# Performance work log

Hardware: AMD Instinct MI355X
Metric: run time of the kernel (lower is better)

The kernel has to match this reference:

```python
import jax, jax.numpy as jnp
import numpy as np

N = 100000
E = 1200000


def _gcn_norm(edge_index, num_nodes):
    # Add self-loops and compute symmetric normalization (PyG GCNConv default).
    row = jnp.concatenate([edge_index[0], jnp.arange(num_nodes, dtype=edge_index.dtype)])
    col = jnp.concatenate([edge_index[1], jnp.arange(num_nodes, dtype=edge_index.dtype)])
    deg = jax.ops.segment_sum(jnp.ones_like(col, dtype=jnp.float32), col, num_segments=num_nodes)
    dinv = jnp.where(deg > 0, jax.lax.rsqrt(jnp.maximum(deg, 1.0)), 0.0)
    norm = dinv[row] * dinv[col]  # [E+N]
    return row, col, norm


def _gcn_conv(x, W, b, row, col, norm, num_nodes):
    h = x @ W                      # [N, out] dense transform first (fewer bytes to gather)
    msg = h[row] * norm[:, None]   # gather + edge-wise scale
    out = jax.ops.segment_sum(msg, col, num_segments=num_nodes)  # scatter-add to targets
    return out + b


def setup_inputs() -> dict:
    key = jax.random.key(0)
    k1, k2, k3, k4 = jax.random.split(key, 4)
    x = jax.random.normal(k1, (N, 128), dtype=jnp.float32)
    edge_index = jax.random.randint(k2, (2, E), 0, N, dtype=jnp.int64)
    W1 = jax.random.normal(k3, (128, 256), dtype=jnp.float32) * (1.0 / np.sqrt(128))
    b1 = jnp.zeros((256,), dtype=jnp.float32)
    W2 = jax.random.normal(k4, (256, 40), dtype=jnp.float32) * (1.0 / np.sqrt(256))
    b2 = jnp.zeros((40,), dtype=jnp.float32)
    return {"x": x, "edge_index": edge_index, "W1": W1, "b1": b1, "W2": W2, "b2": b2}


def reference(x, edge_index, W1, b1, W2, b2):
    row, col, norm = _gcn_norm(edge_index, N)
    h = _gcn_conv(x, W1, b1, row, col, norm, N)
    h = jax.nn.relu(h)
    # dropout omitted: eval mode (training=False) is identity
    return _gcn_conv(h, W2, b2, row, col, norm, N)
```

## Files before the change

### kernel.cpp

```cpp
#include <hip/hip_runtime.h>
#include <hip/hip_bf16.h>

#define NN 100000
#define EE 1200000
#define F1 128
#define F2 256
#define F3 40
#define MROWS 64
#define NBUK ((NN + 255) / 256)
#define NBLK 256
#define CHUNK ((EE + NBLK - 1) / NBLK)
#define DCAP 4096
#define WB ((F1 * F2 + F2 * 48 + 255) / 256)

typedef __bf16 bf16x8 __attribute__((ext_vector_type(8)));
typedef float  f32x4  __attribute__((ext_vector_type(4)));

__device__ __forceinline__ unsigned short f2bf(float f) {
    unsigned u = __float_as_uint(f);
    return (unsigned short)((u + 0x7fffu + ((u >> 16) & 1u)) >> 16);
}
__device__ __forceinline__ float bflo(unsigned v) { return __uint_as_float(v << 16); }
__device__ __forceinline__ float bfhi(unsigned v) { return __uint_as_float(v & 0xffff0000u); }

__global__ __launch_bounds__(256) void k_hist(const int* __restrict__ col,
                                              int* __restrict__ hist) {
    __shared__ int lh[NBUK];
    for (int i = threadIdx.x; i < NBUK; i += 256) lh[i] = 0;
    __syncthreads();
    int e0 = blockIdx.x * CHUNK;
    int e1 = min(e0 + CHUNK, EE);
    for (int e = e0 + threadIdx.x * 4; e + 3 < e1; e += 1024) {
        int4 c = *(const int4*)(col + e);
        if ((unsigned)c.x < (unsigned)NN) atomicAdd(&lh[c.x >> 8], 1);
        if ((unsigned)c.y < (unsigned)NN) atomicAdd(&lh[c.y >> 8], 1);
        if ((unsigned)c.z < (unsigned)NN) atomicAdd(&lh[c.z >> 8], 1);
        if ((unsigned)c.w < (unsigned)NN) atomicAdd(&lh[c.w >> 8], 1);
    }
    __syncthreads();
    for (int i = threadIdx.x; i < NBUK; i += 256) hist[blockIdx.x * NBUK + i] = lh[i];
}

__global__ __launch_bounds__(256) void k_scanbin(int* __restrict__ hist,
                                                 int* __restrict__ bintot) {
    __shared__ int s[NBLK];
    int b = blockIdx.x;
    int v = hist[threadIdx.x * NBUK + b];
    s[threadIdx.x] = v;
    __syncthreads();
    int acc = v;
    for (int d = 1; d < NBLK; d <<= 1) {
        int add = (threadIdx.x >= d) ? s[threadIdx.x - d] : 0;
        __syncthreads();
        acc += add;
        s[threadIdx.x] = acc;
        __syncthreads();
    }
    hist[threadIdx.x * NBUK + b] = acc - v;
    if (threadIdx.x == NBLK - 1) bintot[b] = acc;
}

__global__ __launch_bounds__(512) void k_scanbase(const int* __restrict__ bintot,
                                                  int* __restrict__ binbase) {
    __shared__ int s[512];
    int v = (threadIdx.x < NBUK) ? bintot[threadIdx.x] : 0;
    s[threadIdx.x] = v;
    __syncthreads();
    int acc = v;
    for (int d = 1; d < 512; d <<= 1) {
        int add = (threadIdx.x >= d) ? s[threadIdx.x - d] : 0;
        __syncthreads();
        acc += add;
        s[threadIdx.x] = acc;
        __syncthreads();
    }
    if (threadIdx.x < NBUK) binbase[threadIdx.x] = acc - v;
    if (threadIdx.x == NBUK - 1) binbase[NBUK] = acc;
}

__global__ __launch_bounds__(256) void k_scat(const int* __restrict__ row,
                                              const int* __restrict__ col,
                                              const int* __restrict__ hist,
                                              const int* __restrict__ binbase,
                                              unsigned* __restrict__ rec) {
    __shared__ int lcur[NBUK];
    for (int i = threadIdx.x; i < NBUK; i += 256)
        lcur[i] = binbase[i] + hist[blockIdx.x * NBUK + i];
    __syncthreads();
    int e0 = blockIdx.x * CHUNK;
    int e1 = min(e0 + CHUNK, EE);
    for (int e = e0 + threadIdx.x * 4; e + 3 < e1; e += 1024) {
        int4 r = *(const int4*)(row + e);
        int4 c = *(const int4*)(col + e);
        if ((unsigned)c.x < (unsigned)NN) {
            int p = atomicAdd(&lcur[c.x >> 8], 1);
            rec[p] = ((unsigned)r.x & 0xFFFFFFu) | ((unsigned)(c.x & 255) << 24);
        }
        if ((unsigned)c.y < (unsigned)NN) {
            int p = atomicAdd(&lcur[c.y >> 8], 1);
            rec[p] = ((unsigned)r.y & 0xFFFFFFu) | ((unsigned)(c.y & 255) << 24);
        }
        if ((unsigned)c.z < (unsigned)NN) {
            int p = atomicAdd(&lcur[c.z >> 8], 1);
            rec[p] = ((unsigned)r.z & 0xFFFFFFu) | ((unsigned)(c.z & 255) << 24);
        }
        if ((unsigned)c.w < (unsigned)NN) {
            int p = atomicAdd(&lcur[c.w >> 8], 1);
            rec[p] = ((unsigned)r.w & 0xFFFFFFu) | ((unsigned)(c.w & 255) << 24);
        }
    }
}

__global__ __launch_bounds__(256) void k_csr(const int* __restrict__ binbase,
                                             const unsigned* __restrict__ rec,
                                             int* __restrict__ eidx,
                                             int* __restrict__ cnt,
                                             int* __restrict__ cursor,
                                             float* __restrict__ dinv,
                                             const float4* __restrict__ x4,
                                             unsigned* __restrict__ xh,
                                             const float* __restrict__ W1,
                                             const float* __restrict__ W2,
                                             __hip_bfloat16* __restrict__ W1p,
                                             __hip_bfloat16* __restrict__ W2p) {
    if (blockIdx.x >= NBUK) {
        int idx = (blockIdx.x - NBUK) * 256 + threadIdx.x;
        if (idx < F1 * F2) {
            int k = idx / F2, colw = idx - (idx / F2) * F2;
            int k8 = k >> 3, j = k & 7;
            W1p[((size_t)(k8 * F2 + colw) << 3) + j] = __float2bfloat16(W1[(size_t)k * F2 + colw]);
        } else if (idx < F1 * F2 + F2 * 48) {
            int i2 = idx - F1 * F2;
            int k = i2 / 48, colw = i2 - (i2 / 48) * 48;
            int k8 = k >> 3, j = k & 7;
            float v = (colw < F3) ? W2[(size_t)k * F3 + colw] : 0.0f;
            W2p[((size_t)(k8 * 48 + colw) << 3) + j] = __float2bfloat16(v);
        }
        return;
    }
    __shared__ int lcnt[256];
    __shared__ int s[256];
    __shared__ int lcur[256];
    __shared__ float sdinv[256];
    __shared__ int lde[DCAP];
    const int b = blockIdx.x;
    const int tid = threadIdx.x;
    lcnt[tid] = 0;
    __syncthreads();
    const int base = binbase[b];
    const int nb = min(binbase[b + 1] - base, DCAP);
    for (int j = tid; j < nb; j += 256) atomicAdd(&lcnt[rec[base + j] >> 24], 1);
    __syncthreads();
    int cv = lcnt[tid];
    s[tid] = cv;
    __syncthreads();
    int acc = cv;
    for (int d = 1; d < 256; d <<= 1) {
        int add = (tid >= d) ? s[tid - d] : 0;
        __syncthreads();
        acc += add;
        s[tid] = acc;
        __syncthreads();
    }
    int excl = acc - cv;
    lcur[tid] = excl;
    const int node = (b << 8) + tid;
    float dv = rsqrtf((float)(cv + 1));
    sdinv[tid] = dv;
    if (node < NN) {
        cnt[node] = cv;
        cursor[node] = base + excl + cv;
        dinv[node] = dv;
    }
    __syncthreads();
    for (int j = tid; j < nb; j += 256) {
        unsigned v = rec[base + j];
        int pos = atomicAdd(&lcur[v >> 24], 1);
        lde[pos] = (int)(v & 0xFFFFFFu);
    }
    __syncthreads();
    for (int j = tid; j < nb; j += 256) eidx[base + j] = lde[j];
    for (int j = tid; j < 256 * 32; j += 256) {
        int nl = j >> 5;
        int gn = (b << 8) + nl;
        if (gn < NN) {
            float d = sdinv[nl];
            float4 v = x4[(size_t)gn * 32 + (j & 31)];
            uint2 o;
            o.x = (unsigned)f2bf(v.x * d) | ((unsigned)f2bf(v.y * d) << 16);
            o.y = (unsigned)f2bf(v.z * d) | ((unsigned)f2bf(v.w * d) << 16);
            *(uint2*)(xh + ((size_t)gn << 6) + ((j & 31) << 1)) = o;
        }
    }
}

__global__ __launch_bounds__(256) void k_agg1(const int* __restrict__ cursor,
                                              const int* __restrict__ cnt,
                                              const int* __restrict__ eidx,
                                              const float* __restrict__ dinv,
                                              const unsigned* __restrict__ xh,
                                              unsigned* __restrict__ agg) {
    int node = blockIdx.x * 4 + (threadIdx.x >> 6);
    int lane = threadIdx.x & 63;
    if (node >= NN) return;
    const int g = lane >> 4;
    const int l = lane & 15;
    float a0, a1, a2, a3, a4, a5, a6, a7;
    {
        uint4 v = {0u, 0u, 0u, 0u};
        if (g == 0) v = *(const uint4*)(xh + ((size_t)node << 6) + (l << 2));
        a0 = bflo(v.x); a1 = bfhi(v.x); a2 = bflo(v.y); a3 = bfhi(v.y);
        a4 = bflo(v.z); a5 = bfhi(v.z); a6 = bflo(v.w); a7 = bfhi(v.w);
    }
    int n = cnt[node];
    int s = cursor[node] - n;
    int k = 0;
    for (; k + 7 < n; k += 8) {
        int r0 = eidx[s + k + g];
        int r1 = eidx[s + k + 4 + g];
        uint4 v0 = *(const uint4*)(xh + ((size_t)r0 << 6) + (l << 2));
        uint4 v1 = *(const uint4*)(xh + ((size_t)r1 << 6) + (l << 2));
        a0 += bflo(v0.x); a1 += bfhi(v0.x); a2 += bflo(v0.y); a3 += bfhi(v0.y);
        a4 += bflo(v0.z); a5 += bfhi(v0.z); a6 += bflo(v0.w); a7 += bfhi(v0.w);
        a0 += bflo(v1.x); a1 += bfhi(v1.x); a2 += bflo(v1.y); a3 += bfhi(v1.y);
        a4 += bflo(v1.z); a5 += bfhi(v1.z); a6 += bflo(v1.w); a7 += bfhi(v1.w);
    }
    for (; k < n; k += 4) {
        if (k + g < n) {
            int r0 = eidx[s + k + g];
            uint4 v0 = *(const uint4*)(xh + ((size_t)r0 << 6) + (l << 2));
            a0 += bflo(v0.x); a1 += bfhi(v0.x); a2 += bflo(v0.y); a3 += bfhi(v0.y);
            a4 += bflo(v0.z); a5 += bfhi(v0.z); a6 += bflo(v0.w); a7 += bfhi(v0.w);
        }
    }
    a0 += __shfl_down(a0, 32, 64); a1 += __shfl_down(a1, 32, 64);
    a2 += __shfl_down(a2, 32, 64); a3 += __shfl_down(a3, 32, 64);
    a4 += __shfl_down(a4, 32, 64); a5 += __shfl_down(a5, 32, 64);
    a6 += __shfl_down(a6, 32, 64); a7 += __shfl_down(a7, 32, 64);
    a0 += __shfl_down(a0, 16, 64); a1 += __shfl_down(a1, 16, 64);
    a2 += __shfl_down(a2, 16, 64); a3 += __shfl_down(a3, 16, 64);
    a4 += __shfl_down(a4, 16, 64); a5 += __shfl_down(a5, 16, 64);
    a6 += __shfl_down(a6, 16, 64); a7 += __shfl_down(a7, 16, 64);
    if (g == 0) {
        float d = dinv[node];
        uint4 o;
        o.x = (unsigned)f2bf(a0 * d) | ((unsigned)f2bf(a1 * d) << 16);
        o.y = (unsigned)f2bf(a2 * d) | ((unsigned)f2bf(a3 * d) << 16);
        o.z = (unsigned)f2bf(a4 * d) | ((unsigned)f2bf(a5 * d) << 16);
        o.w = (unsigned)f2bf(a6 * d) | ((unsigned)f2bf(a7 * d) << 16);
        *(uint4*)(agg + ((size_t)node << 6) + (l << 2)) = o;
    }
}

__global__ __launch_bounds__(256) void k_gemm_mfma(
    const __hip_bfloat16* __restrict__ agg, const __hip_bfloat16* __restrict__ W1p,
    const float* __restrict__ b1, const __hip_bfloat16* __restrict__ W2p,
    const float* __restrict__ dinv, unsigned short* __restrict__ tg) {
    __shared__ __hip_bfloat16 h_s[MROWS][F2 + 8];
    const int i0   = blockIdx.x * MROWS;
    const int wave = threadIdx.x >> 6;
    const int lane = threadIdx.x & 63;
    const int m = lane & 15, q = lane >> 4;
    const int rowA = i0 + wave * 16 + m;

    f32x4 acc[16];
#pragma unroll
    for (int c = 0; c < 16; ++c) acc[c] = (f32x4){0.f, 0.f, 0.f, 0.f};

#pragma unroll
    for (int s = 0; s < 4; ++s) {
        bf16x8 a;
#pragma unroll
        for (int j = 0; j < 8; ++j) a[j] = (__bf16)0.0f;
        if (rowA < NN) a = *(const bf16x8*)(agg + (size_t)rowA * F1 + s * 32 + q * 8);
        const __hip_bfloat16* bp = W1p + ((size_t)(4 * s + q) * F2) * 8;
#pragma unroll
        for (int c = 0; c < 16; ++c) {
            bf16x8 b = *(const bf16x8*)(bp + ((size_t)(c * 16 + m) << 3));
            acc[c] = __builtin_amdgcn_mfma_f32_16x16x32_bf16(a, b, acc[c], 0, 0, 0);
        }
    }

#pragma unroll
    for (int c = 0; c < 16; ++c) {
        int col = c * 16 + m;
        float bj = b1[col];
#pragma unroll
        for (int r = 0; r < 4; ++r) {
            int lr = wave * 16 + q * 4 + r;
            h_s[lr][col] = __float2bfloat16(fmaxf(acc[c][r] + bj, 0.0f));
        }
    }
    __syncthreads();

    f32x4 acc2[3];
#pragma unroll
    for (int c = 0; c < 3; ++c) acc2[c] = (f32x4){0.f, 0.f, 0.f, 0.f};

#pragma unroll
    for (int s = 0; s < 8; ++s) {
        bf16x8 a = *(const bf16x8*)(&h_s[wave * 16 + m][s * 32 + q * 8]);
        const __hip_bfloat16* bp = W2p + ((size_t)(4 * s + q) * 48) * 8;
#pragma unroll
        for (int c = 0; c < 3; ++c) {
            bf16x8 b = *(const bf16x8*)(bp + ((size_t)(c * 16 + m) << 3));
            acc2[c] = __builtin_amdgcn_mfma_f32_16x16x32_bf16(a, b, acc2[c], 0, 0, 0);
        }
    }

#pragma unroll
    for (int c = 0; c < 3; ++c) {
        int col = c * 16 + m;
        if (col < F3) {
#pragma unroll
            for (int r = 0; r < 4; ++r) {
                int grow = i0 + wave * 16 + q * 4 + r;
                if (grow < NN)
                    tg[((size_t)grow << 6) + col] = f2bf(acc2[c][r] * dinv[grow]);
            }
        }
    }
}

__global__ __launch_bounds__(256) void k_agg2(const int* __restrict__ cursor,
                                              const int* __restrict__ cnt,
                                              const int* __restrict__ eidx,
                                              const float* __restrict__ dinv,
                                              const unsigned* __restrict__ tg32,
                                              const float* __restrict__ b2,
                                              float* __restrict__ out) {
    int node = blockIdx.x * 4 + (threadIdx.x >> 6);
    int lane = threadIdx.x & 63;
    if (node >= NN) return;
    const int g = lane / 20;
    const int l = lane - g * 20;
    const bool act = g < 3;
    float a0 = 0.f, a1 = 0.f;
    if (g == 0) {
        unsigned v = tg32[((size_t)node << 5) + l];
        a0 = bflo(v); a1 = bfhi(v);
    }
    int n = cnt[node];
    int s = cursor[node] - n;
    int k = 0;
    for (; k + 5 < n; k += 6) {
        unsigned v0 = 0u, v1 = 0u;
        if (act) {
            int r0 = eidx[s + k + g];
            int r1 = eidx[s + k + 3 + g];
            v0 = tg32[((size_t)r0 << 5) + l];
            v1 = tg32[((size_t)r1 << 5) + l];
        }
        a0 += bflo(v0); a1 += bfhi(v0);
        a0 += bflo(v1); a1 += bfhi(v1);
    }
    for (; k < n; k += 3) {
        if (act && (k + g) < n) {
            int r0 = eidx[s + k + g];
            unsigned v0 = tg32[((size_t)r0 << 5) + l];
            a0 += bflo(v0); a1 += bfhi(v0);
        }
    }
    float t0a = __shfl_down(a0, 20, 64), t0b = __shfl_down(a0, 40, 64);
    float t1a = __shfl_down(a1, 20, 64), t1b = __shfl_down(a1, 40, 64);
    if (lane < 20) {
        float d = dinv[node];
        float o0 = d * (a0 + t0a + t0b) + b2[2 * lane];
        float o1 = d * (a1 + t1a + t1b) + b2[2 * lane + 1];
        float2 o = {o0, o1};
        *(float2*)(out + (size_t)node * F3 + (lane << 1)) = o;
    }
}

extern "C" void kernel_launch(void* const* d_in, const int* in_sizes, int n_in,
                              void* d_out, int out_size, void* d_ws, size_t ws_size,
                              hipStream_t stream) {
    const float* x  = (const float*)d_in[0];
    const int*   ei = (const int*)d_in[1];
    const float* W1 = (const float*)d_in[2];
    const float* b1 = (const float*)d_in[3];
    const float* W2 = (const float*)d_in[4];
    const float* b2 = (const float*)d_in[5];
    float* out = (float*)d_out;

    const int* row = ei;
    const int* col = ei + EE;

    int* cnt     = (int*)d_ws;
    int* cursor  = cnt + NN;
    float* dinv  = (float*)(cursor + NN);
    int* hist    = (int*)(dinv + NN);
    int* bintot  = hist + NBLK * NBUK;
    int* binbase = bintot + NBUK;
    int* eidx    = binbase + (NBUK + 1) + 7;
    unsigned* xh  = (unsigned*)(eidx + EE);
    unsigned* agg = xh + (size_t)NN * 64;
    unsigned* rec = agg;
    unsigned short* tg = (unsigned short*)xh;
    __hip_bfloat16* W1p = (__hip_bfloat16*)(agg + (size_t)NN * 64);
    __hip_bfloat16* W2p = W1p + (size_t)F1 * F2;

    k_hist    <<<NBLK, 256, 0, stream>>>(col, hist);
    k_scanbin <<<NBUK, NBLK, 0, stream>>>(hist, bintot);
    k_scanbase<<<1, 512, 0, stream>>>(bintot, binbase);
    k_scat    <<<NBLK, 256, 0, stream>>>(row, col, hist, binbase, rec);
    k_csr     <<<NBUK + WB, 256, 0, stream>>>(binbase, rec, eidx, cnt, cursor, dinv,
                                              (const float4*)x, xh, W1, W2, W1p, W2p);

    k_agg1<<<(NN + 3) / 4, 256, 0, stream>>>(cursor, cnt, eidx, dinv, xh, agg);
    k_gemm_mfma<<<(NN + MROWS - 1) / MROWS, 256, 0, stream>>>(
        (const __hip_bfloat16*)agg, W1p, b1, W2p, dinv, tg);
    k_agg2<<<(NN + 3) / 4, 256, 0, stream>>>(cursor, cnt, eidx, dinv,
                                             (const unsigned*)tg, b2, out);
}
```

Measured before the change: 306.1 us.

## Fuse first-layer aggregation into the MFMA GEMM kernel via shared memory

Merges the layer-1 neighbor aggregation kernel with the two-GEMM MFMA kernel. Each wave now aggregates its 16 rows sequentially into a shared-memory tile, and the GEMMs read that tile instead of a global agg buffer. This removes one launch and a full write and read of the aggregated feature matrix. In exchange, the gather phase runs in far fewer blocks and each wave walks 16 nodes serially, which may reduce memory-level parallelism and occupancy for the latency-bound gather. LDS use per block also goes up.

```diff
diff --git a/kernel.cpp b/kernel.cpp
--- a/kernel.cpp
+++ b/kernel.cpp
@@ -194,85 +194,84 @@
     }
 }
 
-__global__ __launch_bounds__(256) void k_agg1(const int* __restrict__ cursor,
-                                              const int* __restrict__ cnt,
-                                              const int* __restrict__ eidx,
-                                              const float* __restrict__ dinv,
-                                              const unsigned* __restrict__ xh,
-                                              unsigned* __restrict__ agg) {
-    int node = blockIdx.x * 4 + (threadIdx.x >> 6);
-    int lane = threadIdx.x & 63;
-    if (node >= NN) return;
-    const int g = lane >> 4;
-    const int l = lane & 15;
-    float a0, a1, a2, a3, a4, a5, a6, a7;
-    {
-        uint4 v = {0u, 0u, 0u, 0u};
-        if (g == 0) v = *(const uint4*)(xh + ((size_t)node << 6) + (l << 2));
-        a0 = bflo(v.x); a1 = bfhi(v.x); a2 = bflo(v.y); a3 = bfhi(v.y);
-        a4 = bflo(v.z); a5 = bfhi(v.z); a6 = bflo(v.w); a7 = bfhi(v.w);
-    }
-    int n = cnt[node];
-    int s = cursor[node] - n;
-    int k = 0;
-    for (; k + 7 < n; k += 8) {
-        int r0 = eidx[s + k + g];
-        int r1 = eidx[s + k + 4 + g];
-        uint4 v0 = *(const uint4*)(xh + ((size_t)r0 << 6) + (l << 2));
-        uint4 v1 = *(const uint4*)(xh + ((size_t)r1 << 6) + (l << 2));
-        a0 += bflo(v0.x); a1 += bfhi(v0.x); a2 += bflo(v0.y); a3 += bfhi(v0.y);
-        a4 += bflo(v0.z); a5 += bfhi(v0.z); a6 += bflo(v0.w); a7 += bfhi(v0.w);
-        a0 += bflo(v1.x); a1 += bfhi(v1.x); a2 += bflo(v1.y); a3 += bfhi(v1.y);
-        a4 += bflo(v1.z); a5 += bfhi(v1.z); a6 += bflo(v1.w); a7 += bfhi(v1.w);
-    }
-    for (; k < n; k += 4) {
-        if (k + g < n) {
-            int r0 = eidx[s + k + g];
-            uint4 v0 = *(const uint4*)(xh + ((size_t)r0 << 6) + (l << 2));
-            a0 += bflo(v0.x); a1 += bfhi(v0.x); a2 += bflo(v0.y); a3 += bfhi(v0.y);
-            a4 += bflo(v0.z); a5 += bfhi(v0.z); a6 += bflo(v0.w); a7 += bfhi(v0.w);
-        }
-    }
-    a0 += __shfl_down(a0, 32, 64); a1 += __shfl_down(a1, 32, 64);
-    a2 += __shfl_down(a2, 32, 64); a3 += __shfl_down(a3, 32, 64);
-    a4 += __shfl_down(a4, 32, 64); a5 += __shfl_down(a5, 32, 64);
-    a6 += __shfl_down(a6, 32, 64); a7 += __shfl_down(a7, 32, 64);
-    a0 += __shfl_down(a0, 16, 64); a1 += __shfl_down(a1, 16, 64);
-    a2 += __shfl_down(a2, 16, 64); a3 += __shfl_down(a3, 16, 64);
-    a4 += __shfl_down(a4, 16, 64); a5 += __shfl_down(a5, 16, 64);
-    a6 += __shfl_down(a6, 16, 64); a7 += __shfl_down(a7, 16, 64);
-    if (g == 0) {
-        float d = dinv[node];
-        uint4 o;
-        o.x = (unsigned)f2bf(a0 * d) | ((unsigned)f2bf(a1 * d) << 16);
-        o.y = (unsigned)f2bf(a2 * d) | ((unsigned)f2bf(a3 * d) << 16);
-        o.z = (unsigned)f2bf(a4 * d) | ((unsigned)f2bf(a5 * d) << 16);
-        o.w = (unsigned)f2bf(a6 * d) | ((unsigned)f2bf(a7 * d) << 16);
-        *(uint4*)(agg + ((size_t)node << 6) + (l << 2)) = o;
-    }
-}
-
-__global__ __launch_bounds__(256) void k_gemm_mfma(
-    const __hip_bfloat16* __restrict__ agg, const __hip_bfloat16* __restrict__ W1p,
-    const float* __restrict__ b1, const __hip_bfloat16* __restrict__ W2p,
-    const float* __restrict__ dinv, unsigned short* __restrict__ tg) {
+__global__ __launch_bounds__(256) void k_fused(const int* __restrict__ cursor,
+                                               const int* __restrict__ cnt,
+                                               const int* __restrict__ eidx,
+                                               const float* __restrict__ dinv,
+                                               const unsigned* __restrict__ xh,
+                                               const __hip_bfloat16* __restrict__ W1p,
+                                               const float* __restrict__ b1,
+                                               const __hip_bfloat16* __restrict__ W2p,
+                                               unsigned short* __restrict__ tg) {
+    __shared__ __hip_bfloat16 a_s[MROWS][F1 + 8];
     __shared__ __hip_bfloat16 h_s[MROWS][F2 + 8];
     const int i0   = blockIdx.x * MROWS;
     const int wave = threadIdx.x >> 6;
     const int lane = threadIdx.x & 63;
+    const int g = lane >> 4;
+    const int l = lane & 15;
+
+#pragma unroll 1
+    for (int t = 0; t < 16; ++t) {
+        const int node = i0 + (wave << 4) + t;
+        float a0 = 0.f, a1 = 0.f, a2 = 0.f, a3 = 0.f,
+              a4 = 0.f, a5 = 0.f, a6 = 0.f, a7 = 0.f;
+        if (node < NN) {
+            if (g == 0) {
+                uint4 v = *(const uint4*)(xh + ((size_t)node << 6) + (l << 2));
+                a0 = bflo(v.x); a1 = bfhi(v.x); a2 = bflo(v.y); a3 = bfhi(v.y);
+                a4 = bflo(v.z); a5 = bfhi(v.z); a6 = bflo(v.w); a7 = bfhi(v.w);
+            }
+            int n = cnt[node];
+            int s = cursor[node] - n;
+            int k = 0;
+            for (; k + 7 < n; k += 8) {
+                int r0 = eidx[s + k + g];
+                int r1 = eidx[s + k + 4 + g];
+                uint4 v0 = *(const uint4*)(xh + ((size_t)r0 << 6) + (l << 2));
+                uint4 v1 = *(const uint4*)(xh + ((size_t)r1 << 6) + (l << 2));
+                a0 += bflo(v0.x); a1 += bfhi(v0.x); a2 += bflo(v0.y); a3 += bfhi(v0.y);
+                a4 += bflo(v0.z); a5 += bfhi(v0.z); a6 += bflo(v0.w); a7 += bfhi(v0.w);
+                a0 += bflo(v1.x); a1 += bfhi(v1.x); a2 += bflo(v1.y); a3 += bfhi(v1.y);
+                a4 += bflo(v1.z); a5 += bfhi(v1.z); a6 += bflo(v1.w); a7 += bfhi(v1.w);
+            }
+            for (; k < n; k += 4) {
+                if (k + g < n) {
+                    int r0 = eidx[s + k + g];
+                    uint4 v0 = *(const uint4*)(xh + ((size_t)r0 << 6) + (l << 2));
+                    a0 += bflo(v0.x); a1 += bfhi(v0.x); a2 += bflo(v0.y); a3 += bfhi(v0.y);
+                    a4 += bflo(v0.z); a5 += bfhi(v0.z); a6 += bflo(v0.w); a7 += bfhi(v0.w);
+                }
+            }
+        }
+        a0 += __shfl_down(a0, 32, 64); a1 += __shfl_down(a1, 32, 64);
+        a2 += __shfl_down(a2, 32, 64); a3 += __shfl_down(a3, 32, 64);
+        a4 += __shfl_down(a4, 32, 64); a5 += __shfl_down(a5, 32, 64);
+        a6 += __shfl_down(a6, 32, 64); a7 += __shfl_down(a7, 32, 64);
+        a0 += __shfl_down(a0, 16, 64); a1 += __shfl_down(a1, 16, 64);
+        a2 += __shfl_down(a2, 16, 64); a3 += __shfl_down(a3, 16, 64);
+        a4 += __shfl_down(a4, 16, 64); a5 += __shfl_down(a5, 16, 64);
+        a6 += __shfl_down(a6, 16, 64); a7 += __shfl_down(a7, 16, 64);
+        if (g == 0) {
+            float d = (node < NN) ? dinv[node] : 0.0f;
+            uint4 o;
+            o.x = (unsigned)f2bf(a0 * d) | ((unsigned)f2bf(a1 * d) << 16);
+            o.y = (unsigned)f2bf(a2 * d) | ((unsigned)f2bf(a3 * d) << 16);
+            o.z = (unsigned)f2bf(a4 * d) | ((unsigned)f2bf(a5 * d) << 16);
+            o.w = (unsigned)f2bf(a6 * d) | ((unsigned)f2bf(a7 * d) << 16);
+            *(uint4*)(&a_s[(wave << 4) + t][l << 3]) = o;
+        }
+    }
+    __syncthreads();
+
     const int m = lane & 15, q = lane >> 4;
-    const int rowA = i0 + wave * 16 + m;
-
     f32x4 acc[16];
 #pragma unroll
     for (int c = 0; c < 16; ++c) acc[c] = (f32x4){0.f, 0.f, 0.f, 0.f};
 
 #pragma unroll
     for (int s = 0; s < 4; ++s) {
-        bf16x8 a;
-#pragma unroll
-        for (int j = 0; j < 8; ++j) a[j] = (__bf16)0.0f;
-        if (rowA < NN) a = *(const bf16x8*)(agg + (size_t)rowA * F1 + s * 32 + q * 8);
+        bf16x8 a = *(const bf16x8*)(&a_s[(wave << 4) + m][s * 32 + q * 8]);
         const __hip_bfloat16* bp = W1p + ((size_t)(4 * s + q) * F2) * 8;
 #pragma unroll
         for (int c = 0; c < 16; ++c) {
@@ -287,7 +286,7 @@
         float bj = b1[col];
 #pragma unroll
         for (int r = 0; r < 4; ++r) {
-            int lr = wave * 16 + q * 4 + r;
+            int lr = (wave << 4) + q * 4 + r;
             h_s[lr][col] = __float2bfloat16(fmaxf(acc[c][r] + bj, 0.0f));
         }
     }
@@ -299,7 +298,7 @@
 
 #pragma unroll
     for (int s = 0; s < 8; ++s) {
-        bf16x8 a = *(const bf16x8*)(&h_s[wave * 16 + m][s * 32 + q * 8]);
+        bf16x8 a = *(const bf16x8*)(&h_s[(wave << 4) + m][s * 32 + q * 8]);
         const __hip_bfloat16* bp = W2p + ((size_t)(4 * s + q) * 48) * 8;
 #pragma unroll
         for (int c = 0; c < 3; ++c) {
@@ -314,7 +313,7 @@
         if (col < F3) {
 #pragma unroll
             for (int r = 0; r < 4; ++r) {
-                int grow = i0 + wave * 16 + q * 4 + r;
+                int grow = i0 + (wave << 4) + q * 4 + r;
                 if (grow < NN)
                     tg[((size_t)grow << 6) + col] = f2bf(acc2[c][r] * dinv[grow]);
             }
@@ -393,11 +392,10 @@
     int* bintot  = hist + NBLK * NBUK;
     int* binbase = bintot + NBUK;
     int* eidx    = binbase + (NBUK + 1) + 7;
-    unsigned* xh  = (unsigned*)(eidx + EE);
-    unsigned* agg = xh + (size_t)NN * 64;
-    unsigned* rec = agg;
-    unsigned short* tg = (unsigned short*)xh;
-    __hip_bfloat16* W1p = (__hip_bfloat16*)(agg + (size_t)NN * 64);
+    unsigned* xh = (unsigned*)(eidx + EE);
+    unsigned short* tg = (unsigned short*)(xh + (size_t)NN * 64);
+    unsigned* rec = (unsigned*)tg;
+    __hip_bfloat16* W1p = (__hip_bfloat16*)(tg + (size_t)NN * 64);
     __hip_bfloat16* W2p = W1p + (size_t)F1 * F2;
 
     k_hist    <<<NBLK, 256, 0, stream>>>(col, hist);
@@ -407,9 +405,8 @@
     k_csr     <<<NBUK + WB, 256, 0, stream>>>(binbase, rec, eidx, cnt, cursor, dinv,
                                               (const float4*)x, xh, W1, W2, W1p, W2p);
 
-    k_agg1<<<(NN + 3) / 4, 256, 0, stream>>>(cursor, cnt, eidx, dinv, xh, agg);
-    k_gemm_mfma<<<(NN + MROWS - 1) / MROWS, 256, 0, stream>>>(
-        (const __hip_bfloat16*)agg, W1p, b1, W2p, dinv, tg);
+    k_fused<<<(NN + MROWS - 1) / MROWS, 256, 0, stream>>>(
+        cursor, cnt, eidx, dinv, xh, W1p, b1, W2p, tg);
     k_agg2<<<(NN + 3) / 4, 256, 0, stream>>>(cursor, cnt, eidx, dinv,
                                              (const unsigned*)tg, b2, out);
 }
```

Measured after the change: 393.5 us. 28.6% more time.
